# Kernel tuning notes

Hardware: AMD Instinct MI355X
Metric: run time of the kernel (lower is better)

The kernel has to match this reference:

```python
import jax, jax.numpy as jnp
from jax import lax
import numpy as np

UNITS, S, B, T = 64, 16, 512, 4096
LOG_2PI = float(np.log(2.0 * np.pi))


def setup_inputs() -> dict:
    key = jax.random.key(0)
    k1, k2 = jax.random.split(key)
    inputs = jax.random.normal(k1, (B, T), dtype=jnp.float32)
    # positive 'probs' (TFP Categorical takes log internally)
    hmm_params = jax.random.uniform(k2, (UNITS, S, S), dtype=jnp.float32,
                                    minval=1e-3, maxval=1.0)
    return {"inputs": inputs, "hmm_params": hmm_params}


def reference(inputs, hmm_params):
    # --- HMM parameters, as TFP builds them ---
    trans = hmm_params[0]                      # (S, S) unnormalized probs
    log_A = jnp.log(trans) - jnp.log(trans.sum(-1, keepdims=True))  # (S,S) row-normalized
    init = hmm_params[0, 0]                    # (S,)
    log_pi = jnp.log(init) - jnp.log(init.sum())
    # Emission: Normal(loc=0, scale=1) per state -> same logp for every state
    emit = -0.5 * inputs * inputs - 0.5 * LOG_2PI   # [B, T]
    emit = emit[:, :, None]                          # [B, T, 1] broadcasts over S

    # --- Viterbi forward (max-product) ---
    delta0 = log_pi[None, :] + emit[:, 0]            # [B, S]
    emit_seq = jnp.moveaxis(emit[:, 1:], 1, 0)       # [T-1, B, 1]

    def step(delta, e_t):
        scores = delta[:, :, None] + log_A[None, :, :]   # [B, S_prev, S_cur]
        psi = jnp.argmax(scores, axis=1).astype(jnp.int32)  # [B, S]
        delta_new = jnp.max(scores, axis=1) + e_t            # [B, S]
        return delta_new, psi

    deltaT, psis = lax.scan(step, delta0, emit_seq)  # psis: [T-1, B, S]

    # --- Backtrace ---
    zT = jnp.argmax(deltaT, axis=-1).astype(jnp.int32)   # [B]

    def back(z, psi):
        z_prev = jnp.take_along_axis(psi, z[:, None], axis=1)[:, 0]
        return z_prev, z_prev

    _, zs = lax.scan(back, zT, psis, reverse=True)   # zs: [T-1, B] = states t=0..T-2
    path = jnp.concatenate([zs.T, zT[:, None]], axis=1)  # [B, T]
    return path
```

## Files before the change

kernel.cpp:

```cpp
#include <hip/hip_runtime.h>
#include <math.h>

#define T_LEN 4096
#define B_SZ  512

__device__ __forceinline__ float emis(float xv) {
    float a = __fmul_rn(-0.5f, xv);
    float b = __fmul_rn(a, xv);
    return __fsub_rn(b, (float)0.9189385332046727);
}

#define DPP_ROR0(K, SRC) __builtin_amdgcn_update_dpp(0, (SRC), 0x120 + (K), 0xF, 0xF, false)
#define M3(x, y, z) fmaxf(fmaxf(x, y), z)

#define ADDPP(DST, K)                                                                 \
    asm("v_add_f32_dpp %0, %1, %2 row_ror:" #K " row_mask:0xf bank_mask:0xf"          \
        : "=v"(DST) : "v"(d), "v"(a[K]))

#define STEPC(ET)                                                                     \
    {                                                                                 \
        float s0 = __fadd_rn(d, a[0]);                                                \
        float s1, s2, s3, s4, s5, s6, s7, s8, s9, s10, s11, s12, s13, s14, s15;       \
        ADDPP(s1, 1);   ADDPP(s2, 2);   ADDPP(s3, 3);   ADDPP(s4, 4);                 \
        ADDPP(s5, 5);   ADDPP(s6, 6);   ADDPP(s7, 7);   ADDPP(s8, 8);                 \
        ADDPP(s9, 9);   ADDPP(s10, 10); ADDPP(s11, 11); ADDPP(s12, 12);               \
        ADDPP(s13, 13); ADDPP(s14, 14); ADDPP(s15, 15);                               \
        float u0 = M3(s0, s1, s2),  u1 = M3(s3, s4, s5),  u2 = M3(s6, s7, s8);        \
        float u3 = M3(s9, s10, s11), u4 = M3(s12, s13, s14);                          \
        float m = fmaxf(M3(u0, u1, u2), M3(u3, u4, s15));                             \
        d = __fadd_rn(m, ET);                                                         \
    }

#define GRP4(QV, SLOTDW)                                                              \
    {                                                                                 \
        float4 dq;                                                                    \
        STEPC(QV.x) dq.x = d; STEPC(QV.y) dq.y = d;                                   \
        STEPC(QV.z) dq.z = d; STEPC(QV.w) dq.w = d;                                   \
        *(float4*)(db + (SLOTDW)) = dq;                                               \
    }

#define PERMSEL(V, Q)                                                                 \
    {                                                                                 \
        int sel_ = (V) & 7;                                                           \
        int lo_, hi_;                                                                 \
        asm("v_perm_b32 %0, %1, %2, %3" : "=v"(lo_) : "v"((Q).y), "v"((Q).x), "v"(sel_)); \
        asm("v_perm_b32 %0, %1, %2, %3" : "=v"(hi_) : "v"((Q).w), "v"((Q).z), "v"(sel_)); \
        V = (((V) & 8) ? hi_ : lo_) & 0xff;                                           \
    }

#define WALK64(BASE, CUR, PRE, POST)                                                  \
    {                                                                                 \
        uint4 m_[8];                                                                  \
        _Pragma("unroll") for (int z_ = 0; z_ < 8; ++z_)                              \
            m_[z_] = *(const uint4*)((BASE) + (63 - z_) * 16);                        \
        for (int r_ = 63; r_ >= 15; r_ -= 8) {                                        \
            uint4 n_[8];                                                              \
            _Pragma("unroll") for (int z_ = 0; z_ < 8; ++z_)                          \
                n_[z_] = *(const uint4*)((BASE) + (r_ - 8 - z_) * 16);                \
            _Pragma("unroll") for (int z_ = 0; z_ < 8; ++z_) {                        \
                PRE(r_ - z_, CUR) PERMSEL(CUR, m_[z_]) POST(r_ - z_, CUR)             \
            }                                                                         \
            _Pragma("unroll") for (int z_ = 0; z_ < 8; ++z_) m_[z_] = n_[z_];         \
        }                                                                             \
        _Pragma("unroll") for (int z_ = 0; z_ < 8; ++z_) {                            \
            PRE(7 - z_, CUR) PERMSEL(CUR, m_[z_]) POST(7 - z_, CUR)                   \
        }                                                                             \
    }

#define NIBHOP(V, Q) (V) = (int)(((Q) >> ((unsigned)(V) << 2)) & 15ull);

#define NWALK64(BASE, CUR, POST)                                                      \
    {                                                                                 \
        const unsigned long long* bb_ = (BASE);                                       \
        unsigned long long m_[8];                                                     \
        _Pragma("unroll") for (int z_ = 0; z_ < 8; ++z_) m_[z_] = bb_[63 - z_];       \
        for (int r_ = 63; r_ >= 15; r_ -= 8) {                                       \
            unsigned long long n_[8];                                                 \
            _Pragma("unroll") for (int z_ = 0; z_ < 8; ++z_) n_[z_] = bb_[r_ - 8 - z_]; \
            _Pragma("unroll") for (int z_ = 0; z_ < 8; ++z_) {                        \
                NIBHOP(CUR, m_[z_]) POST(r_ - z_, CUR)                                \
            }                                                                         \
            _Pragma("unroll") for (int z_ = 0; z_ < 8; ++z_) m_[z_] = n_[z_];         \
        }                                                                             \
        _Pragma("unroll") for (int z_ = 0; z_ < 8; ++z_) {                            \
            NIBHOP(CUR, m_[z_]) POST(7 - z_, CUR)                                     \
        }                                                                             \
    }

#define NOPX(r, c)
#define EBL_PRE(r, c) eb[r] = (unsigned char)(c);
#define OUT_POST(r, c) ob[r] = (c);

#define RLF(V, L) __int_as_float(__builtin_amdgcn_readlane(__float_as_int(V), (L)))

#define PSI_I(I, V, BL)                                                               \
    {                                                                                 \
        float s_ = __fadd_rn(dd[I], RLF(V, (BL) + (I)));                              \
        if (s_ > best) arg = I;                              \
        best = fmaxf(best, s_);                                                       \
    }

#define PSI_J(JJ, V)                                                                  \
    {                                                                                 \
        float best = __fadd_rn(dd[0], RLF(V, (((JJ) & 3) * 16) + 0));                 \
        int arg = 0;                                                                  \
        PSI_I(1, V, ((JJ) & 3) * 16)  PSI_I(2, V, ((JJ) & 3) * 16)                    \
        PSI_I(3, V, ((JJ) & 3) * 16)  PSI_I(4, V, ((JJ) & 3) * 16)                    \
        PSI_I(5, V, ((JJ) & 3) * 16)  PSI_I(6, V, ((JJ) & 3) * 16)                    \
        PSI_I(7, V, ((JJ) & 3) * 16)  PSI_I(8, V, ((JJ) & 3) * 16)                    \
        PSI_I(9, V, ((JJ) & 3) * 16)  PSI_I(10, V, ((JJ) & 3) * 16)                   \
        PSI_I(11, V, ((JJ) & 3) * 16) PSI_I(12, V, ((JJ) & 3) * 16)                   \
        PSI_I(13, V, ((JJ) & 3) * 16) PSI_I(14, V, ((JJ) & 3) * 16)                   \
        PSI_I(15, V, ((JJ) & 3) * 16)                                                 \
        pk |= (unsigned long long)arg << ((JJ) * 4);                                  \
    }

__global__ __launch_bounds__(256) void k_fused(const float* __restrict__ x,
                                               const float* __restrict__ hmm,
                                               int* __restrict__ out) {
    __shared__ __align__(16) float dbuf[2][2][16][68];
    __shared__ unsigned long long pnib[2][64 * 65];
    __shared__ uint4 Mlv[2][64];
    __shared__ unsigned char Ebl[2][64];
    __shared__ float carry_l[2][16];
    __shared__ float logA_l[256];
    __shared__ float logAT_l[256];
    __shared__ __align__(16) float Ebuf[4][2][64];

    const int tid = threadIdx.x;
    const int wave = tid >> 6;
    const int blk = blockIdx.x;

    {
        const int pi = tid >> 4, pj = tid & 15;
        const float* row = hmm + pi * 16;
        float r8[8];
#pragma unroll
        for (int k = 0; k < 8; ++k) r8[k] = __fadd_rn(row[k], row[k + 8]);
        float s = __fadd_rn(
            __fadd_rn(__fadd_rn(r8[0], r8[1]), __fadd_rn(r8[2], r8[3])),
            __fadd_rn(__fadd_rn(r8[4], r8[5]), __fadd_rn(r8[6], r8[7])));
        float la = (float)log((double)row[pj]);
        float ls = (float)log((double)s);
        float v = __fsub_rn(la, ls);
        logA_l[tid] = v;
        logAT_l[pj * 16 + pi] = v;
        const int cc0 = tid >> 7, gp = (tid >> 6) & 1, l0 = tid & 63;
        Ebuf[cc0][gp][l0] = emis(x[(size_t)(blk * 2 + gp) * T_LEN + 64 * cc0 + l0 + 1]);
    }
    __syncthreads();

    if (wave == 0) {
        asm volatile("s_setprio 3");
        const int j = tid & 15, g = tid >> 4;
        float a[16];
        float d = 0.f;
        float4 q0, q1, q2, q3;
        if (g < 2) {
            a[0] = logA_l[j * 16 + j];
#define LOADA(K) { int sk = DPP_ROR0(K, j); a[K] = logA_l[sk * 16 + j]; }
            LOADA(1)  LOADA(2)  LOADA(3)  LOADA(4)  LOADA(5)
            LOADA(6)  LOADA(7)  LOADA(8)  LOADA(9)  LOADA(10)
            LOADA(11) LOADA(12) LOADA(13) LOADA(14) LOADA(15)
#undef LOADA
            const int b = blk * 2 + g;
            float e0 = emis(x[(size_t)b * T_LEN]);
            d = __fadd_rn(logA_l[j], e0);
            const float4* e0p = (const float4*)&Ebuf[0][g][0];
            q0 = e0p[0]; q1 = e0p[1]; q2 = e0p[2]; q3 = e0p[3];
        }
        for (int p = 0; p < 66; ++p) {
            __syncthreads();
            if (p < 64 && g < 2) {
                float* db = &dbuf[p & 1][g][j][0];
                db[64] = d;
                const float4* ecur = (const float4*)&Ebuf[p & 3][g][0];
                const float4* enxt = (const float4*)&Ebuf[(p + 1) & 3][g][0];
                if (p < 63) {
#pragma clang loop unroll(disable)
                    for (int ii = 0; ii < 3; ++ii) {
                        GRP4(q0, ii * 16 + 0)  q0 = ecur[(ii + 1) * 4 + 0];
                        GRP4(q1, ii * 16 + 4)  q1 = ecur[(ii + 1) * 4 + 1];
                        GRP4(q2, ii * 16 + 8)  q2 = ecur[(ii + 1) * 4 + 2];
                        GRP4(q3, ii * 16 + 12) q3 = ecur[(ii + 1) * 4 + 3];
                    }
                    GRP4(q0, 48) q0 = enxt[0];
                    GRP4(q1, 52) q1 = enxt[1];
                    GRP4(q2, 56) q2 = enxt[2];
                    GRP4(q3, 60) q3 = enxt[3];
                } else {
#pragma clang loop unroll(disable)
                    for (int ii = 0; ii < 3; ++ii) {
                        GRP4(q0, ii * 16 + 0)  q0 = ecur[(ii + 1) * 4 + 0];
                        GRP4(q1, ii * 16 + 4)  q1 = ecur[(ii + 1) * 4 + 1];
                        GRP4(q2, ii * 16 + 8)  q2 = ecur[(ii + 1) * 4 + 2];
                        GRP4(q3, ii * 16 + 12) q3 = ecur[(ii + 1) * 4 + 3];
                    }
                    GRP4(q0, 48) GRP4(q1, 52) GRP4(q2, 56)
                    STEPC(q3.x) db[60] = d;
                    STEPC(q3.y) db[61] = d;
                    STEPC(q3.z) db[62] = d;
                }
            }
        }
        if (g < 2) carry_l[g][j] = d;
    } else if (wave <= 2) {
        const int g2 = wave - 1;
        const int r = tid & 63;
        float vq0 = logAT_l[r];
        float vq1 = logAT_l[64 + r];
        float vq2 = logAT_l[128 + r];
        float vq3 = logAT_l[192 + r];
        for (int p = 0; p < 66; ++p) {
            __syncthreads();
            const int c = p - 1;
            if (c >= 0 && c < 64) {
                const int t2 = 64 * c + 1 + r;
                if (t2 <= T_LEN - 1) {
                    const int q = c & 1;
                    const int rs = (r == 0) ? 64 : (r - 1);
                    float dd[16];
#pragma unroll
                    for (int i = 0; i < 16; ++i) dd[i] = dbuf[q][g2][i][rs];
                    asm volatile("" : "+v"(vq0), "+v"(vq1), "+v"(vq2), "+v"(vq3));
                    unsigned long long pk = 0ull;
                    PSI_J(0, vq0)  PSI_J(1, vq0)  PSI_J(2, vq0)  PSI_J(3, vq0)
                    PSI_J(4, vq1)  PSI_J(5, vq1)  PSI_J(6, vq1)  PSI_J(7, vq1)
                    PSI_J(8, vq2)  PSI_J(9, vq2)  PSI_J(10, vq2) PSI_J(11, vq2)
                    PSI_J(12, vq3) PSI_J(13, vq3) PSI_J(14, vq3) PSI_J(15, vq3)
                    pnib[g2][c * 65 + r] = pk;
                } else {
                    pnib[g2][c * 65 + 63] = 0xFEDCBA9876543210ull;
                }
            }
        }
    } else {
        const int l = tid - 192;
        const int g3 = l >> 4, z = l & 15;
        for (int p = 0; p < 66; ++p) {
            __syncthreads();
            const int cc = p + 2;
            if (cc < 64) {
                const int t = 64 * cc + l + 1;
                if (t <= T_LEN - 1) {
                    Ebuf[cc & 3][0][l] = emis(x[(size_t)(blk * 2 + 0) * T_LEN + t]);
                    Ebuf[cc & 3][1][l] = emis(x[(size_t)(blk * 2 + 1) * T_LEN + t]);
                }
            }
            const int c = p - 2;
            if (c >= 0 && l < 32) {
                int cur = z;
                NWALK64(&pnib[g3][c * 65], cur, NOPX)
                ((unsigned char*)&Mlv[g3][c])[z] = (unsigned char)cur;
            }
        }
    }

    __syncthreads();
    if (tid < 2) {
        const int g = tid;
        float best = carry_l[g][0]; int zT = 0;
#pragma unroll
        for (int i = 1; i < 16; ++i) {
            float s = carry_l[g][i];
            if (s > best) zT = i;
            best = fmaxf(best, s);
        }
        int z = zT;
        unsigned char* eb = &Ebl[g][0];
        WALK64((const unsigned char*)&Mlv[g][0], z, EBL_PRE, NOPX)
    }
    __syncthreads();
    if (tid < 128) {
        const int g = tid >> 6, c = tid & 63;
        int* ob = out + (size_t)(blk * 2 + g) * T_LEN + c * 64;
        int cur = Ebl[g][c];
        NWALK64(&pnib[g][c * 65], cur, OUT_POST)
    }
}

extern "C" void kernel_launch(void* const* d_in, const int* in_sizes, int n_in,
                              void* d_out, int out_size, void* d_ws, size_t ws_size,
                              hipStream_t stream) {
    (void)in_sizes; (void)n_in; (void)out_size; (void)d_ws; (void)ws_size;
    const float* x   = (const float*)d_in[0];
    const float* hmm = (const float*)d_in[1];
    int* out = (int*)d_out;

    hipLaunchKernelGGL(k_fused, dim3(B_SZ / 2), dim3(256), 0, stream, x, hmm, out);
}
```

Before: 294.0 us.

## Double chunk length to 128 steps, halving barrier phases

Chunks grow from 64 to 128 timesteps, so the pipelined phase loop runs 34 iterations instead of 66 and needs about half as many __syncthreads barriers. The psi waves now handle two timesteps per lane and share each readlane of the transition column between them. The emission loader fills two entries per lane per phase. The costs are longer serial work per phase for the delta wave, longer per-chunk backtrace walks, only 64 threads doing the final output walk, and more shared memory.

```diff
diff --git a/kernel.cpp b/kernel.cpp
--- a/kernel.cpp
+++ b/kernel.cpp
@@ -3,6 +3,10 @@
 
 #define T_LEN 4096
 #define B_SZ  512
+#define CH    128
+#define NCH   32
+#define PITCH 129
+#define PHASES 34
 
 __device__ __forceinline__ float emis(float xv) {
     float a = __fmul_rn(-0.5f, xv);
@@ -48,12 +52,12 @@
         V = (((V) & 8) ? hi_ : lo_) & 0xff;                                           \
     }
 
-#define WALK64(BASE, CUR, PRE, POST)                                                  \
+#define WALKN(BASE, CUR, PRE, POST, START)                                            \
     {                                                                                 \
         uint4 m_[8];                                                                  \
         _Pragma("unroll") for (int z_ = 0; z_ < 8; ++z_)                              \
-            m_[z_] = *(const uint4*)((BASE) + (63 - z_) * 16);                        \
-        for (int r_ = 63; r_ >= 15; r_ -= 8) {                                        \
+            m_[z_] = *(const uint4*)((BASE) + ((START) - z_) * 16);                   \
+        for (int r_ = (START); r_ >= 15; r_ -= 8) {                                   \
             uint4 n_[8];                                                              \
             _Pragma("unroll") for (int z_ = 0; z_ < 8; ++z_)                          \
                 n_[z_] = *(const uint4*)((BASE) + (r_ - 8 - z_) * 16);                \
@@ -69,12 +73,12 @@
 
 #define NIBHOP(V, Q) (V) = (int)(((Q) >> ((unsigned)(V) << 2)) & 15ull);
 
-#define NWALK64(BASE, CUR, POST)                                                      \
+#define NWALKN(BASE, CUR, POST, START)                                                \
     {                                                                                 \
         const unsigned long long* bb_ = (BASE);                                       \
         unsigned long long m_[8];                                                     \
-        _Pragma("unroll") for (int z_ = 0; z_ < 8; ++z_) m_[z_] = bb_[63 - z_];       \
-        for (int r_ = 63; r_ >= 15; r_ -= 8) {                                       \
+        _Pragma("unroll") for (int z_ = 0; z_ < 8; ++z_) m_[z_] = bb_[(START) - z_];  \
+        for (int r_ = (START); r_ >= 15; r_ -= 8) {                                   \
             unsigned long long n_[8];                                                 \
             _Pragma("unroll") for (int z_ = 0; z_ < 8; ++z_) n_[z_] = bb_[r_ - 8 - z_]; \
             _Pragma("unroll") for (int z_ = 0; z_ < 8; ++z_) {                        \
@@ -93,39 +97,45 @@
 
 #define RLF(V, L) __int_as_float(__builtin_amdgcn_readlane(__float_as_int(V), (L)))
 
-#define PSI_I(I, V, BL)                                                               \
-    {                                                                                 \
-        float s_ = __fadd_rn(dd[I], RLF(V, (BL) + (I)));                              \
-        if (s_ > best) arg = I;                              \
-        best = fmaxf(best, s_);                                                       \
-    }
-
-#define PSI_J(JJ, V)                                                                  \
-    {                                                                                 \
-        float best = __fadd_rn(dd[0], RLF(V, (((JJ) & 3) * 16) + 0));                 \
-        int arg = 0;                                                                  \
-        PSI_I(1, V, ((JJ) & 3) * 16)  PSI_I(2, V, ((JJ) & 3) * 16)                    \
-        PSI_I(3, V, ((JJ) & 3) * 16)  PSI_I(4, V, ((JJ) & 3) * 16)                    \
-        PSI_I(5, V, ((JJ) & 3) * 16)  PSI_I(6, V, ((JJ) & 3) * 16)                    \
-        PSI_I(7, V, ((JJ) & 3) * 16)  PSI_I(8, V, ((JJ) & 3) * 16)                    \
-        PSI_I(9, V, ((JJ) & 3) * 16)  PSI_I(10, V, ((JJ) & 3) * 16)                   \
-        PSI_I(11, V, ((JJ) & 3) * 16) PSI_I(12, V, ((JJ) & 3) * 16)                   \
-        PSI_I(13, V, ((JJ) & 3) * 16) PSI_I(14, V, ((JJ) & 3) * 16)                   \
-        PSI_I(15, V, ((JJ) & 3) * 16)                                                 \
-        pk |= (unsigned long long)arg << ((JJ) * 4);                                  \
+#define PSI2_I(I, V, BL)                                                              \
+    {                                                                                 \
+        float cs_ = RLF(V, (BL) + (I));                                               \
+        float sA_ = __fadd_rn(ddA[I], cs_);                                           \
+        if (sA_ > bestA) argA = I;                           \
+        bestA = fmaxf(bestA, sA_);                                                    \
+        float sB_ = __fadd_rn(ddB[I], cs_);                                           \
+        if (sB_ > bestB) argB = I;                                                    \
+        bestB = fmaxf(bestB, sB_);                                                    \
+    }
+
+#define PSI2_J(JJ, V)                                                                 \
+    {                                                                                 \
+        float c0_ = RLF(V, (((JJ) & 3) * 16) + 0);                                    \
+        float bestA = __fadd_rn(ddA[0], c0_); int argA = 0;                           \
+        float bestB = __fadd_rn(ddB[0], c0_); int argB = 0;                           \
+        PSI2_I(1, V, ((JJ) & 3) * 16)  PSI2_I(2, V, ((JJ) & 3) * 16)                  \
+        PSI2_I(3, V, ((JJ) & 3) * 16)  PSI2_I(4, V, ((JJ) & 3) * 16)                  \
+        PSI2_I(5, V, ((JJ) & 3) * 16)  PSI2_I(6, V, ((JJ) & 3) * 16)                  \
+        PSI2_I(7, V, ((JJ) & 3) * 16)  PSI2_I(8, V, ((JJ) & 3) * 16)                  \
+        PSI2_I(9, V, ((JJ) & 3) * 16)  PSI2_I(10, V, ((JJ) & 3) * 16)                 \
+        PSI2_I(11, V, ((JJ) & 3) * 16) PSI2_I(12, V, ((JJ) & 3) * 16)                 \
+        PSI2_I(13, V, ((JJ) & 3) * 16) PSI2_I(14, V, ((JJ) & 3) * 16)                 \
+        PSI2_I(15, V, ((JJ) & 3) * 16)                                                \
+        pkA |= (unsigned long long)argA << ((JJ) * 4);                                \
+        pkB |= (unsigned long long)argB << ((JJ) * 4);                                \
     }
 
 __global__ __launch_bounds__(256) void k_fused(const float* __restrict__ x,
                                                const float* __restrict__ hmm,
                                                int* __restrict__ out) {
-    __shared__ __align__(16) float dbuf[2][2][16][68];
-    __shared__ unsigned long long pnib[2][64 * 65];
-    __shared__ uint4 Mlv[2][64];
-    __shared__ unsigned char Ebl[2][64];
+    __shared__ __align__(16) float dbuf[2][2][16][132];
+    __shared__ unsigned long long pnib[2][NCH * PITCH];
+    __shared__ uint4 Mlv[2][NCH];
+    __shared__ unsigned char Ebl[2][NCH];
     __shared__ float carry_l[2][16];
     __shared__ float logA_l[256];
     __shared__ float logAT_l[256];
-    __shared__ __align__(16) float Ebuf[4][2][64];
+    __shared__ __align__(16) float Ebuf[4][2][CH];
 
     const int tid = threadIdx.x;
     const int wave = tid >> 6;
@@ -146,7 +156,9 @@
         logA_l[tid] = v;
         logAT_l[pj * 16 + pi] = v;
         const int cc0 = tid >> 7, gp = (tid >> 6) & 1, l0 = tid & 63;
-        Ebuf[cc0][gp][l0] = emis(x[(size_t)(blk * 2 + gp) * T_LEN + 64 * cc0 + l0 + 1]);
+        const size_t xb = (size_t)(blk * 2 + gp) * T_LEN + CH * cc0 + l0 + 1;
+        Ebuf[cc0][gp][l0]      = emis(x[xb]);
+        Ebuf[cc0][gp][l0 + 64] = emis(x[xb + 64]);
     }
     __syncthreads();
 
@@ -169,37 +181,37 @@
             const float4* e0p = (const float4*)&Ebuf[0][g][0];
             q0 = e0p[0]; q1 = e0p[1]; q2 = e0p[2]; q3 = e0p[3];
         }
-        for (int p = 0; p < 66; ++p) {
+        for (int p = 0; p < PHASES; ++p) {
             __syncthreads();
-            if (p < 64 && g < 2) {
+            if (p < NCH && g < 2) {
                 float* db = &dbuf[p & 1][g][j][0];
-                db[64] = d;
+                db[128] = d;
                 const float4* ecur = (const float4*)&Ebuf[p & 3][g][0];
                 const float4* enxt = (const float4*)&Ebuf[(p + 1) & 3][g][0];
-                if (p < 63) {
+                if (p < NCH - 1) {
 #pragma clang loop unroll(disable)
-                    for (int ii = 0; ii < 3; ++ii) {
+                    for (int ii = 0; ii < 7; ++ii) {
                         GRP4(q0, ii * 16 + 0)  q0 = ecur[(ii + 1) * 4 + 0];
                         GRP4(q1, ii * 16 + 4)  q1 = ecur[(ii + 1) * 4 + 1];
                         GRP4(q2, ii * 16 + 8)  q2 = ecur[(ii + 1) * 4 + 2];
                         GRP4(q3, ii * 16 + 12) q3 = ecur[(ii + 1) * 4 + 3];
                     }
-                    GRP4(q0, 48) q0 = enxt[0];
-                    GRP4(q1, 52) q1 = enxt[1];
-                    GRP4(q2, 56) q2 = enxt[2];
-                    GRP4(q3, 60) q3 = enxt[3];
+                    GRP4(q0, 112) q0 = enxt[0];
+                    GRP4(q1, 116) q1 = enxt[1];
+                    GRP4(q2, 120) q2 = enxt[2];
+                    GRP4(q3, 124) q3 = enxt[3];
                 } else {
 #pragma clang loop unroll(disable)
-                    for (int ii = 0; ii < 3; ++ii) {
+                    for (int ii = 0; ii < 7; ++ii) {
                         GRP4(q0, ii * 16 + 0)  q0 = ecur[(ii + 1) * 4 + 0];
                         GRP4(q1, ii * 16 + 4)  q1 = ecur[(ii + 1) * 4 + 1];
                         GRP4(q2, ii * 16 + 8)  q2 = ecur[(ii + 1) * 4 + 2];
                         GRP4(q3, ii * 16 + 12) q3 = ecur[(ii + 1) * 4 + 3];
                     }
-                    GRP4(q0, 48) GRP4(q1, 52) GRP4(q2, 56)
-                    STEPC(q3.x) db[60] = d;
-                    STEPC(q3.y) db[61] = d;
-                    STEPC(q3.z) db[62] = d;
+                    GRP4(q0, 112) GRP4(q1, 116) GRP4(q2, 120)
+                    STEPC(q3.x) db[124] = d;
+                    STEPC(q3.y) db[125] = d;
+                    STEPC(q3.z) db[126] = d;
                 }
             }
         }
@@ -211,46 +223,50 @@
         float vq1 = logAT_l[64 + r];
         float vq2 = logAT_l[128 + r];
         float vq3 = logAT_l[192 + r];
-        for (int p = 0; p < 66; ++p) {
+        for (int p = 0; p < PHASES; ++p) {
             __syncthreads();
             const int c = p - 1;
-            if (c >= 0 && c < 64) {
-                const int t2 = 64 * c + 1 + r;
-                if (t2 <= T_LEN - 1) {
-                    const int q = c & 1;
-                    const int rs = (r == 0) ? 64 : (r - 1);
-                    float dd[16];
+            if (c >= 0 && c < NCH) {
+                const int q = c & 1;
+                const int rsA = (r == 0) ? 128 : (r - 1);
+                const int rsB = r + 63;
+                float ddA[16], ddB[16];
 #pragma unroll
-                    for (int i = 0; i < 16; ++i) dd[i] = dbuf[q][g2][i][rs];
-                    asm volatile("" : "+v"(vq0), "+v"(vq1), "+v"(vq2), "+v"(vq3));
-                    unsigned long long pk = 0ull;
-                    PSI_J(0, vq0)  PSI_J(1, vq0)  PSI_J(2, vq0)  PSI_J(3, vq0)
-                    PSI_J(4, vq1)  PSI_J(5, vq1)  PSI_J(6, vq1)  PSI_J(7, vq1)
-                    PSI_J(8, vq2)  PSI_J(9, vq2)  PSI_J(10, vq2) PSI_J(11, vq2)
-                    PSI_J(12, vq3) PSI_J(13, vq3) PSI_J(14, vq3) PSI_J(15, vq3)
-                    pnib[g2][c * 65 + r] = pk;
-                } else {
-                    pnib[g2][c * 65 + 63] = 0xFEDCBA9876543210ull;
+                for (int i = 0; i < 16; ++i) {
+                    ddA[i] = dbuf[q][g2][i][rsA];
+                    ddB[i] = dbuf[q][g2][i][rsB];
                 }
+                asm volatile("" : "+v"(vq0), "+v"(vq1), "+v"(vq2), "+v"(vq3));
+                unsigned long long pkA = 0ull, pkB = 0ull;
+                PSI2_J(0, vq0)  PSI2_J(1, vq0)  PSI2_J(2, vq0)  PSI2_J(3, vq0)
+                PSI2_J(4, vq1)  PSI2_J(5, vq1)  PSI2_J(6, vq1)  PSI2_J(7, vq1)
+                PSI2_J(8, vq2)  PSI2_J(9, vq2)  PSI2_J(10, vq2) PSI2_J(11, vq2)
+                PSI2_J(12, vq3) PSI2_J(13, vq3) PSI2_J(14, vq3) PSI2_J(15, vq3)
+                if (c == NCH - 1 && r == 63) pkB = 0xFEDCBA9876543210ull;
+                pnib[g2][c * PITCH + r]      = pkA;
+                pnib[g2][c * PITCH + r + 64] = pkB;
             }
         }
     } else {
         const int l = tid - 192;
         const int g3 = l >> 4, z = l & 15;
-        for (int p = 0; p < 66; ++p) {
+        for (int p = 0; p < PHASES; ++p) {
             __syncthreads();
             const int cc = p + 2;
-            if (cc < 64) {
-                const int t = 64 * cc + l + 1;
-                if (t <= T_LEN - 1) {
-                    Ebuf[cc & 3][0][l] = emis(x[(size_t)(blk * 2 + 0) * T_LEN + t]);
-                    Ebuf[cc & 3][1][l] = emis(x[(size_t)(blk * 2 + 1) * T_LEN + t]);
+            if (cc < NCH) {
+                const int t1 = CH * cc + l + 1;
+                const int t2 = t1 + 64;
+                Ebuf[cc & 3][0][l] = emis(x[(size_t)(blk * 2 + 0) * T_LEN + t1]);
+                Ebuf[cc & 3][1][l] = emis(x[(size_t)(blk * 2 + 1) * T_LEN + t1]);
+                if (t2 <= T_LEN - 1) {
+                    Ebuf[cc & 3][0][l + 64] = emis(x[(size_t)(blk * 2 + 0) * T_LEN + t2]);
+                    Ebuf[cc & 3][1][l + 64] = emis(x[(size_t)(blk * 2 + 1) * T_LEN + t2]);
                 }
             }
             const int c = p - 2;
             if (c >= 0 && l < 32) {
                 int cur = z;
-                NWALK64(&pnib[g3][c * 65], cur, NOPX)
+                NWALKN(&pnib[g3][c * PITCH], cur, NOPX, 127)
                 ((unsigned char*)&Mlv[g3][c])[z] = (unsigned char)cur;
             }
         }
@@ -268,14 +284,14 @@
         }
         int z = zT;
         unsigned char* eb = &Ebl[g][0];
-        WALK64((const unsigned char*)&Mlv[g][0], z, EBL_PRE, NOPX)
+        WALKN((const unsigned char*)&Mlv[g][0], z, EBL_PRE, NOPX, NCH - 1)
     }
     __syncthreads();
-    if (tid < 128) {
-        const int g = tid >> 6, c = tid & 63;
-        int* ob = out + (size_t)(blk * 2 + g) * T_LEN + c * 64;
+    if (tid < 64) {
+        const int g = tid >> 5, c = tid & 31;
+        int* ob = out + (size_t)(blk * 2 + g) * T_LEN + c * CH;
         int cur = Ebl[g][c];
-        NWALK64(&pnib[g][c * 65], cur, OUT_POST)
+        NWALKN(&pnib[g][c * PITCH], cur, OUT_POST, 127)
     }
 }
 
```

Measured after the change: 289.3 us (median of 2 runs). About the same (-1.6%).
